# Kernel optimization log

Hardware: AMD Instinct MI355X
Metric: run time of the kernel (lower is better)

The kernel has to match this reference:

```python
import jax, jax.numpy as jnp
import numpy as np

K_OUT = 16  # k_out
DT = 0.1    # integration interval t=[0.0, 0.1], single rk4 step


def setup_inputs() -> dict:
    key = jax.random.key(0)
    ks = jax.random.split(key, 12)
    B, K_H, K_IN_TOT = 32768, 1024, 256
    s = 0.02
    return {
        "state": jax.random.normal(ks[0], (B, K_OUT + K_H), jnp.float32),
        "xt": jax.random.normal(ks[1], (B, K_IN_TOT), jnp.float32),
        "W1": jax.random.normal(ks[2], (K_H, 2 * K_H), jnp.float32) * s,
        "b1": jnp.zeros((2 * K_H,), jnp.float32),
        "W2": jax.random.normal(ks[3], (2 * K_H, K_H), jnp.float32) * s,
        "b2": jnp.zeros((K_H,), jnp.float32),
        "Wih": jax.random.normal(ks[4], (3 * K_H, K_IN_TOT), jnp.float32) * s,
        "Whh": jax.random.normal(ks[5], (3 * K_H, K_H), jnp.float32) * s,
        "bih": jnp.zeros((3 * K_H,), jnp.float32),
        "bhh": jnp.zeros((3 * K_H,), jnp.float32),
        "Wly": jax.random.normal(ks[6], (K_H, K_OUT), jnp.float32) * s,
        "bly": jnp.zeros((K_OUT,), jnp.float32),
        "y_type": jnp.zeros((K_OUT,), jnp.int32),  # 'd'/'s'/'n' all map to 0
    }


def _ode_f(h, W1, b1, W2, b2):
    # ODE_Rnn_Func: Linear -> Tanh -> Linear (time-independent)
    return jnp.tanh(h @ W1 + b1) @ W2 + b2


def _rk4_step(h, dt, W1, b1, W2, b2):
    k1 = _ode_f(h, W1, b1, W2, b2)
    k2 = _ode_f(h + 0.5 * dt * k1, W1, b1, W2, b2)
    k3 = _ode_f(h + 0.5 * dt * k2, W1, b1, W2, b2)
    k4 = _ode_f(h + dt * k3, W1, b1, W2, b2)
    return h + (dt / 6.0) * (k1 + 2.0 * k2 + 2.0 * k3 + k4)


def _gru_cell(x, h, Wih, Whh, bih, bhh):
    gi = x @ Wih.T + bih  # [B, 3*K_H]
    gh = h @ Whh.T + bhh
    i_r, i_z, i_n = jnp.split(gi, 3, axis=-1)
    h_r, h_z, h_n = jnp.split(gh, 3, axis=-1)
    r = jax.nn.sigmoid(i_r + h_r)
    z = jax.nn.sigmoid(i_z + h_z)
    n = jnp.tanh(i_n + r * h_n)
    return (1.0 - z) * n + z * h


def reference(state, xt, W1, b1, W2, b2, Wih, Whh, bih, bhh, Wly, bly, y_type):
    yt, ht = state[..., :K_OUT], state[..., K_OUT:]
    ht_ = _rk4_step(ht, DT, W1, b1, W2, b2)       # odeint(func, ht, [0, 0.1], method='rk4')[1]
    ht_new = _gru_cell(xt, ht_, Wih, Whh, bih, bhh)
    ly_out = ht_new @ Wly + bly                   # [B, K_OUT]
    mask = (y_type == 0)                          # all True for 'd'/'s'/'n'
    yt_new = jnp.where(mask, ly_out, yt)
    return jnp.concatenate([yt_new, ht_new], axis=-1)
```

## Files before the change

### kernel.cpp

```cpp
#include <hip/hip_runtime.h>
#include <hip/hip_fp8.h>
#include <cstdint>
#include <cstddef>

typedef __bf16 bf16_t;
typedef unsigned char fp8_t;
typedef __attribute__((ext_vector_type(8))) __bf16 bf16x8;
typedef __attribute__((ext_vector_type(4))) float f32x4;

__device__ __forceinline__ void async_cp16(const void* g, void* l) {
    __builtin_amdgcn_global_load_lds(
        (const __attribute__((address_space(1))) void*)g,
        (__attribute__((address_space(3))) void*)l,
        16, 0, 0);
}

__device__ __forceinline__ fp8_t to_fp8(float x) {
    __hip_fp8_e4m3 t(x);
    return t.__x;
}

__device__ __forceinline__ float fast_tanh(float x) {
    float ax = fabsf(x);
    float e = __expf(-2.f * ax);
    float t = (1.f - e) / (1.f + e);
    return x < 0.f ? -t : t;
}
__device__ __forceinline__ float fast_sig(float x) {
    return 1.f / (1.f + __expf(-x));
}

__global__ void k_cvt_transpose8(const float* __restrict__ src, fp8_t* __restrict__ dst,
                                 int K, int N) {
    int idx = blockIdx.x * 256 + threadIdx.x;
    if (idx >= K * N) return;
    int k = idx / N, n = idx - k * N;
    dst[(size_t)n * K + k] = to_fp8(src[idx]);
}

__global__ void k_cvt_flat(const float* __restrict__ src, bf16_t* __restrict__ dst, int n) {
    int idx = blockIdx.x * 256 + threadIdx.x;
    if (idx >= n) return;
    dst[idx] = (bf16_t)src[idx];
}

__global__ void k_build_wrz(const float* __restrict__ Wih, const float* __restrict__ Whh,
                            const float* __restrict__ bih, const float* __restrict__ bhh,
                            bf16_t* __restrict__ wrz, float* __restrict__ brz) {
    int idx = blockIdx.x * 256 + threadIdx.x;
    if (idx >= 2048 * 1280) return;
    int n = idx / 1280, c = idx - n * 1280;
    float v = (c < 256) ? Wih[(size_t)n * 256 + c] : Whh[(size_t)n * 1024 + (c - 256)];
    wrz[idx] = (bf16_t)v;
    if (c == 0) brz[n] = bih[n] + bhh[n];
}

__global__ void k_cvt_inputs(const float* __restrict__ xt, const float* __restrict__ state,
                             bf16_t* __restrict__ xh, bf16_t* __restrict__ h0b,
                             fp8_t* __restrict__ hs8, int B) {
    int idx = blockIdx.x * 256 + threadIdx.x;
    if (idx >= B * 1280) return;
    int b = idx / 1280, c = idx - b * 1280;
    if (c < 256) {
        xh[(size_t)b * 1280 + c] = (bf16_t)xt[(size_t)b * 256 + c];
    } else {
        int j = c - 256;
        float v = state[(size_t)b * 1040 + 16 + j];
        h0b[(size_t)b * 1024 + j] = (bf16_t)v;
        hs8[(size_t)b * 1024 + j] = to_fp8(v);
    }
}

enum { EPI_TANH = 0, EPI_RK4 = 1, EPI_SIG = 2, EPI_BIASBF = 3, EPI_FIN = 4 };

template <int EPI, int STAGE>
__global__ __launch_bounds__(512, 4) void gemm128f8(
    const fp8_t* __restrict__ A, int lda,
    const fp8_t* __restrict__ Bt,
    int N, int K,
    const float* __restrict__ bias,
    fp8_t* __restrict__ o8,
    const bf16_t* __restrict__ h0b,
    const float* __restrict__ state,
    bf16_t* __restrict__ kacc,
    bf16_t* __restrict__ xhb)
{
    __shared__ __align__(16) fp8_t dsA[3][8192];
    __shared__ __align__(16) fp8_t dsB[3][16384];

    const int tid  = threadIdx.x;
    const int lane = tid & 63;
    const int wv   = tid >> 6;

    const int gx  = gridDim.x;
    int bid = blockIdx.y * gx + blockIdx.x;
    const int nwg = gx * gridDim.y;
    bid = (bid & 7) * (nwg >> 3) + (bid >> 3);
    const int bm = (bid / gx) << 7;
    const int bn = (bid % gx) << 8;

    const int wm = (wv >> 2) << 6;
    const int wn = (wv & 3) << 6;

    f32x4 acc[4][4] = {};

    const int srow = tid >> 2;
    const int s4   = tid & 3;
    const int scol = ((s4 ^ ((srow >> 1) & 3)) << 4);
    const fp8_t* gA0 = A  + (size_t)(bm + srow) * lda + scol;
    const fp8_t* gB0 = Bt + (size_t)(bn + srow) * K + scol;
    const fp8_t* gB1 = gB0 + (size_t)128 * K;
    const int d0 = tid << 4;

#define STG(t) do { const int _sl = (t) % 3; const size_t _o = (size_t)(t) << 6; \
        async_cp16(gA0 + _o, (void*)&dsA[_sl][d0]);                              \
        async_cp16(gB0 + _o, (void*)&dsB[_sl][d0]);                              \
        async_cp16(gB1 + _o, (void*)&dsB[_sl][8192 + d0]); } while (0)

    const int fr  = lane & 15;
    const int kg  = lane >> 4;
    const int mS  = ((fr >> 1) & 3) << 1;
    const int aRow = (wm + fr) * 64;
    const int bRow = (wn + fr) * 64;
    const int sk0 = ((kg ^ mS) & 7) << 3;
    const int sk1 = (((4 | kg) ^ mS) & 7) << 3;

    const int NT = K >> 6;

    STG(0);
    STG(1);

    for (int kt = 0; kt < NT; ++kt) {
        if (kt + 1 < NT) asm volatile("s_waitcnt vmcnt(3)" ::: "memory");
        else             asm volatile("s_waitcnt vmcnt(0)" ::: "memory");
        __builtin_amdgcn_s_barrier();

        if (kt + 2 < NT) STG(kt + 2);

        const fp8_t* as = dsA[kt % 3];
        const fp8_t* bs = dsB[kt % 3];
        long a0[4], a1[4], b0[4], b1[4];
#pragma unroll
        for (int i = 0; i < 4; ++i) {
            a0[i] = *(const long*)(as + aRow + i * 1024 + sk0);
            a1[i] = *(const long*)(as + aRow + i * 1024 + sk1);
        }
#pragma unroll
        for (int j = 0; j < 4; ++j) {
            b0[j] = *(const long*)(bs + bRow + j * 1024 + sk0);
            b1[j] = *(const long*)(bs + bRow + j * 1024 + sk1);
        }

        __builtin_amdgcn_s_setprio(1);
#pragma unroll
        for (int i = 0; i < 4; ++i)
#pragma unroll
            for (int j = 0; j < 4; ++j)
                acc[i][j] = __builtin_amdgcn_mfma_f32_16x16x32_fp8_fp8(
                    a0[i], b0[j], acc[i][j], 0, 0, 0);
#pragma unroll
        for (int i = 0; i < 4; ++i)
#pragma unroll
            for (int j = 0; j < 4; ++j)
                acc[i][j] = __builtin_amdgcn_mfma_f32_16x16x32_fp8_fp8(
                    a1[i], b1[j], acc[i][j], 0, 0, 0);
        __builtin_amdgcn_s_setprio(0);
    }
#undef STG

    const int orow0 = bm + wm + (kg << 2);
    const int ocol0 = bn + wn + fr;
#pragma unroll
    for (int i = 0; i < 4; ++i) {
#pragma unroll
        for (int j = 0; j < 4; ++j) {
#pragma unroll
            for (int r = 0; r < 4; ++r) {
                const int row = orow0 + i * 16 + r;
                const int col = ocol0 + j * 16;
                const float c = acc[i][j][r];
                if constexpr (EPI == EPI_TANH) {
                    o8[(size_t)row * N + col] = to_fp8(fast_tanh(c + bias[col]));
                } else {
                    const float kk = c + bias[col];
                    const size_t hidx = ((size_t)row << 10) + col;
                    if constexpr (STAGE == 0) {
                        const float h0 = (float)h0b[hidx];
                        kacc[hidx] = (bf16_t)kk;
                        o8[hidx] = to_fp8(h0 + 0.05f * kk);
                    } else if constexpr (STAGE == 1) {
                        const float h0 = (float)h0b[hidx];
                        kacc[hidx] = (bf16_t)((float)kacc[hidx] + 2.f * kk);
                        o8[hidx] = to_fp8(h0 + 0.05f * kk);
                    } else if constexpr (STAGE == 2) {
                        const float h0 = (float)h0b[hidx];
                        kacc[hidx] = (bf16_t)((float)kacc[hidx] + 2.f * kk);
                        o8[hidx] = to_fp8(h0 + 0.1f * kk);
                    } else {
                        const float h0 = state[(size_t)row * 1040 + 16 + col];
                        const float ht = h0 + (0.1f / 6.f) * ((float)kacc[hidx] + kk);
                        xhb[(size_t)row * 1280 + col] = (bf16_t)ht;
                    }
                }
            }
        }
    }
}

template <int EPI>
__global__ __launch_bounds__(512, 4) void gemm128bf(
    const bf16_t* __restrict__ A, int lda,
    const bf16_t* __restrict__ Bt,
    int N, int K,
    const float* __restrict__ bias,
    bf16_t* __restrict__ o16,
    const bf16_t* __restrict__ rz,
    const bf16_t* __restrict__ inb,
    float* __restrict__ outp)
{
    __shared__ __align__(16) bf16_t As[3][4096];
    __shared__ __align__(16) bf16_t Bs[3][8192];

    const int tid  = threadIdx.x;
    const int lane = tid & 63;
    const int wv   = tid >> 6;

    const int gx  = gridDim.x;
    int bid = blockIdx.y * gx + blockIdx.x;
    const int nwg = gx * gridDim.y;
    if ((nwg & 7) == 0) bid = (bid & 7) * (nwg >> 3) + (bid >> 3);
    const int bm = (bid / gx) << 7;
    const int bn = (bid % gx) << 8;

    const int wm = (wv >> 2) << 6;
    const int wn = (wv & 3) << 6;

    f32x4 acc[4][4] = {};

    const int srow = tid >> 2;
    const int s4   = tid & 3;
    const int scw  = (s4 ^ ((srow >> 1) & 3)) << 3;
    const bf16_t* gA0 = A  + (size_t)(bm + srow) * lda + scw;
    const bf16_t* gB0 = Bt + (size_t)(bn + srow) * K + scw;
    const bf16_t* gB1 = gB0 + (size_t)128 * K;
    const int ldsOff = tid << 3;

#define STG(t) do { const int _sl = (t) % 3; const size_t _o = (size_t)(t) << 5; \
        async_cp16(gA0 + _o, (void*)&As[_sl][ldsOff]);                           \
        async_cp16(gB0 + _o, (void*)&Bs[_sl][ldsOff]);                           \
        async_cp16(gB1 + _o, (void*)&Bs[_sl][4096 + ldsOff]); } while (0)

    const int fr = lane & 15;
    const int kg = lane >> 4;
    const int ra = wm + fr;
    const int rb = wn + fr;
    const int aoff0 = ra * 32 + ((kg ^ ((ra >> 1) & 3)) << 3);
    const int boff0 = rb * 32 + ((kg ^ ((rb >> 1) & 3)) << 3);

    const int NT = K >> 5;

    STG(0);
    STG(1);

    for (int kt = 0; kt < NT; ++kt) {
        if (kt + 1 < NT) asm volatile("s_waitcnt vmcnt(3)" ::: "memory");
        else             asm volatile("s_waitcnt vmcnt(0)" ::: "memory");
        __builtin_amdgcn_s_barrier();

        if (kt + 2 < NT) STG(kt + 2);

        const bf16_t* as = &As[kt % 3][0];
        const bf16_t* bs = &Bs[kt % 3][0];
        bf16x8 af[4], bfr[4];
#pragma unroll
        for (int i = 0; i < 4; ++i) af[i]  = *(const bf16x8*)(as + aoff0 + i * 512);
#pragma unroll
        for (int j = 0; j < 4; ++j) bfr[j] = *(const bf16x8*)(bs + boff0 + j * 512);

        __builtin_amdgcn_s_setprio(1);
#pragma unroll
        for (int i = 0; i < 4; ++i)
#pragma unroll
            for (int j = 0; j < 4; ++j)
                acc[i][j] = __builtin_amdgcn_mfma_f32_16x16x32_bf16(af[i], bfr[j], acc[i][j], 0, 0, 0);
        __builtin_amdgcn_s_setprio(0);
    }
#undef STG

    const int orow0 = bm + wm + (kg << 2);
    const int ocol0 = bn + wn + fr;
#pragma unroll
    for (int i = 0; i < 4; ++i) {
#pragma unroll
        for (int j = 0; j < 4; ++j) {
#pragma unroll
            for (int r = 0; r < 4; ++r) {
                const int row = orow0 + i * 16 + r;
                const int col = ocol0 + j * 16;
                const float c = acc[i][j][r];
                if constexpr (EPI == EPI_SIG) {
                    o16[(size_t)row * N + col] = (bf16_t)fast_sig(c + bias[col]);
                } else if constexpr (EPI == EPI_BIASBF) {
                    o16[(size_t)row * N + col] = (bf16_t)(c + bias[col]);
                } else {
                    const float hn  = c + bias[col];
                    const float r_  = (float)rz[((size_t)row << 11) + col];
                    const float z_  = (float)rz[((size_t)row << 11) + 1024 + col];
                    const float inv = (float)inb[((size_t)row << 10) + col];
                    const float nn  = fast_tanh(inv + r_ * hn);
                    const float htv = (float)A[(size_t)row * lda + col];
                    outp[(size_t)row * 1040 + 16 + col] = (1.f - z_) * nn + z_ * htv;
                }
            }
        }
    }
}

__global__ void k_ly(const float* __restrict__ outh, const float* __restrict__ state,
                     const float* __restrict__ Wly, const float* __restrict__ bly,
                     const int* __restrict__ y_type, float* __restrict__ outp, int B) {
    int t = blockIdx.x * 256 + threadIdx.x;
    if (t >= B * 16) return;
    int o = t & 15, b = t >> 4;
    const float4* hrow = (const float4*)(outh + (size_t)b * 1040 + 16);
    float s = bly[o];
#pragma unroll 4
    for (int k4 = 0; k4 < 256; ++k4) {
        float4 h = hrow[k4];
        int k = k4 << 2;
        s += h.x * Wly[(k + 0) * 16 + o] + h.y * Wly[(k + 1) * 16 + o]
           + h.z * Wly[(k + 2) * 16 + o] + h.w * Wly[(k + 3) * 16 + o];
    }
    outp[(size_t)b * 1040 + o] = (y_type[o] == 0) ? s : state[(size_t)b * 1040 + o];
}

extern "C" void kernel_launch(void* const* d_in, const int* in_sizes, int n_in,
                              void* d_out, int out_size, void* d_ws, size_t ws_size,
                              hipStream_t stream) {
    const float* state = (const float*)d_in[0];
    const float* xt    = (const float*)d_in[1];
    const float* W1    = (const float*)d_in[2];
    const float* b1    = (const float*)d_in[3];
    const float* W2    = (const float*)d_in[4];
    const float* b2    = (const float*)d_in[5];
    const float* Wih   = (const float*)d_in[6];
    const float* Whh   = (const float*)d_in[7];
    const float* bih   = (const float*)d_in[8];
    const float* bhh   = (const float*)d_in[9];
    const float* Wly   = (const float*)d_in[10];
    const float* bly   = (const float*)d_in[11];
    const int*   y_type = (const int*)d_in[12];
    float* out = (float*)d_out;

    const int B = in_sizes[0] / 1040;

    char* ws = (char*)d_ws;
    fp8_t*  w1t8 = (fp8_t*) (ws);
    fp8_t*  w2t8 = (fp8_t*) (ws + 2097152);
    bf16_t* wrz  = (bf16_t*)(ws + 4194304);
    bf16_t* win  = (bf16_t*)(ws + 9437184);
    bf16_t* whn  = (bf16_t*)(ws + 9961472);
    float*  brz  = (float*) (ws + 12058624);
    bf16_t* xh   = (bf16_t*)(ws + 12066816);
    fp8_t*  hs8  = (fp8_t*) (ws + 95952896);
    bf16_t* kacc = (bf16_t*)(ws + 129507328);
    fp8_t*  T8   = (fp8_t*) (ws + 196616192);
    bf16_t* h0b  = (bf16_t*)(ws + 263725056);
    bf16_t* rz   = (bf16_t*)(ws + 196616192);
    bf16_t* inb  = (bf16_t*)(ws + 95952896);

    k_cvt_transpose8<<<(1024 * 2048) / 256, 256, 0, stream>>>(W1, w1t8, 1024, 2048);
    k_cvt_transpose8<<<(2048 * 1024) / 256, 256, 0, stream>>>(W2, w2t8, 2048, 1024);
    k_build_wrz<<<(2048 * 1280) / 256, 256, 0, stream>>>(Wih, Whh, bih, bhh, wrz, brz);
    k_cvt_flat<<<(1024 * 256) / 256, 256, 0, stream>>>(Wih + 2048 * 256, win, 1024 * 256);
    k_cvt_flat<<<(1024 * 1024) / 256, 256, 0, stream>>>(Whh + 2048 * 1024, whn, 1024 * 1024);
    k_cvt_inputs<<<(B * 1280) / 256, 256, 0, stream>>>(xt, state, xh, h0b, hs8, B);

    const int MB = B / 128;

    gemm128f8<EPI_TANH, 0><<<dim3(8, MB), 512, 0, stream>>>(hs8, 1024, w1t8, 2048, 1024,
        b1, T8, nullptr, nullptr, nullptr, nullptr);
    gemm128f8<EPI_RK4, 0><<<dim3(4, MB), 512, 0, stream>>>(T8, 2048, w2t8, 1024, 2048,
        b2, hs8, h0b, nullptr, kacc, nullptr);

    gemm128f8<EPI_TANH, 0><<<dim3(8, MB), 512, 0, stream>>>(hs8, 1024, w1t8, 2048, 1024,
        b1, T8, nullptr, nullptr, nullptr, nullptr);
    gemm128f8<EPI_RK4, 1><<<dim3(4, MB), 512, 0, stream>>>(T8, 2048, w2t8, 1024, 2048,
        b2, hs8, h0b, nullptr, kacc, nullptr);

    gemm128f8<EPI_TANH, 0><<<dim3(8, MB), 512, 0, stream>>>(hs8, 1024, w1t8, 2048, 1024,
        b1, T8, nullptr, nullptr, nullptr, nullptr);
    gemm128f8<EPI_RK4, 2><<<dim3(4, MB), 512, 0, stream>>>(T8, 2048, w2t8, 1024, 2048,
        b2, hs8, h0b, nullptr, kacc, nullptr);

    gemm128f8<EPI_TANH, 0><<<dim3(8, MB), 512, 0, stream>>>(hs8, 1024, w1t8, 2048, 1024,
        b1, T8, nullptr, nullptr, nullptr, nullptr);
    gemm128f8<EPI_RK4, 3><<<dim3(4, MB), 512, 0, stream>>>(T8, 2048, w2t8, 1024, 2048,
        b2, nullptr, nullptr, state, kacc, xh + 256);

    gemm128bf<EPI_SIG><<<dim3(8, MB), 512, 0, stream>>>(xh, 1280, wrz, 2048, 1280,
        brz, rz, nullptr, nullptr, nullptr);
    gemm128bf<EPI_BIASBF><<<dim3(4, MB), 512, 0, stream>>>(xh, 1280, win, 1024, 256,
        bih + 2048, inb, nullptr, nullptr, nullptr);
    gemm128bf<EPI_FIN><<<dim3(4, MB), 512, 0, stream>>>(xh + 256, 1280, whn, 1024, 1024,
        bhh + 2048, nullptr, rz, inb, out);

    k_ly<<<(B * 16) / 256, 256, 0, stream>>>(out, state, Wly, bly, y_type, out, B);
}
```

Before: 1.852 ms.

## Grow GEMM block tile to 256x256 with 1024-thread workgroups

Both the FP8 and BF16 GEMM kernels move from 128x256 tiles with 512 threads to 256x256 tiles with 1024 threads (16 waves). The A staging buffer doubles and each thread now issues one A and one B async copy per stage, so the vmcnt wait drops from 3 to 2. The aim is more operand reuse per tile and less global/L2 traffic for the B matrix. The trade-off is twice the LDS per block, which lowers how many blocks fit on a CU, and only half as many blocks across the grid. The launch_bounds occupancy hint of 4 blocks per CU is unlikely to be met at 1024 threads.

```diff
diff --git a/kernel.cpp b/kernel.cpp
--- a/kernel.cpp
+++ b/kernel.cpp
@@ -74,7 +74,7 @@
 enum { EPI_TANH = 0, EPI_RK4 = 1, EPI_SIG = 2, EPI_BIASBF = 3, EPI_FIN = 4 };
 
 template <int EPI, int STAGE>
-__global__ __launch_bounds__(512, 4) void gemm128f8(
+__global__ __launch_bounds__(1024, 4) void gemm256f8(
     const fp8_t* __restrict__ A, int lda,
     const fp8_t* __restrict__ Bt,
     int N, int K,
@@ -85,7 +85,7 @@
     bf16_t* __restrict__ kacc,
     bf16_t* __restrict__ xhb)
 {
-    __shared__ __align__(16) fp8_t dsA[3][8192];
+    __shared__ __align__(16) fp8_t dsA[3][16384];
     __shared__ __align__(16) fp8_t dsB[3][16384];
 
     const int tid  = threadIdx.x;
@@ -96,7 +96,7 @@
     int bid = blockIdx.y * gx + blockIdx.x;
     const int nwg = gx * gridDim.y;
     bid = (bid & 7) * (nwg >> 3) + (bid >> 3);
-    const int bm = (bid / gx) << 7;
+    const int bm = (bid / gx) << 8;
     const int bn = (bid % gx) << 8;
 
     const int wm = (wv >> 2) << 6;
@@ -109,13 +109,11 @@
     const int scol = ((s4 ^ ((srow >> 1) & 3)) << 4);
     const fp8_t* gA0 = A  + (size_t)(bm + srow) * lda + scol;
     const fp8_t* gB0 = Bt + (size_t)(bn + srow) * K + scol;
-    const fp8_t* gB1 = gB0 + (size_t)128 * K;
     const int d0 = tid << 4;
 
 #define STG(t) do { const int _sl = (t) % 3; const size_t _o = (size_t)(t) << 6; \
         async_cp16(gA0 + _o, (void*)&dsA[_sl][d0]);                              \
-        async_cp16(gB0 + _o, (void*)&dsB[_sl][d0]);                              \
-        async_cp16(gB1 + _o, (void*)&dsB[_sl][8192 + d0]); } while (0)
+        async_cp16(gB0 + _o, (void*)&dsB[_sl][d0]); } while (0)
 
     const int fr  = lane & 15;
     const int kg  = lane >> 4;
@@ -131,7 +129,7 @@
     STG(1);
 
     for (int kt = 0; kt < NT; ++kt) {
-        if (kt + 1 < NT) asm volatile("s_waitcnt vmcnt(3)" ::: "memory");
+        if (kt + 1 < NT) asm volatile("s_waitcnt vmcnt(2)" ::: "memory");
         else             asm volatile("s_waitcnt vmcnt(0)" ::: "memory");
         __builtin_amdgcn_s_barrier();
 
@@ -208,7 +206,7 @@
 }
 
 template <int EPI>
-__global__ __launch_bounds__(512, 4) void gemm128bf(
+__global__ __launch_bounds__(1024, 4) void gemm256bf(
     const bf16_t* __restrict__ A, int lda,
     const bf16_t* __restrict__ Bt,
     int N, int K,
@@ -218,7 +216,7 @@
     const bf16_t* __restrict__ inb,
     float* __restrict__ outp)
 {
-    __shared__ __align__(16) bf16_t As[3][4096];
+    __shared__ __align__(16) bf16_t As[3][8192];
     __shared__ __align__(16) bf16_t Bs[3][8192];
 
     const int tid  = threadIdx.x;
@@ -229,7 +227,7 @@
     int bid = blockIdx.y * gx + blockIdx.x;
     const int nwg = gx * gridDim.y;
     if ((nwg & 7) == 0) bid = (bid & 7) * (nwg >> 3) + (bid >> 3);
-    const int bm = (bid / gx) << 7;
+    const int bm = (bid / gx) << 8;
     const int bn = (bid % gx) << 8;
 
     const int wm = (wv >> 2) << 6;
@@ -242,13 +240,11 @@
     const int scw  = (s4 ^ ((srow >> 1) & 3)) << 3;
     const bf16_t* gA0 = A  + (size_t)(bm + srow) * lda + scw;
     const bf16_t* gB0 = Bt + (size_t)(bn + srow) * K + scw;
-    const bf16_t* gB1 = gB0 + (size_t)128 * K;
     const int ldsOff = tid << 3;
 
 #define STG(t) do { const int _sl = (t) % 3; const size_t _o = (size_t)(t) << 5; \
         async_cp16(gA0 + _o, (void*)&As[_sl][ldsOff]);                           \
-        async_cp16(gB0 + _o, (void*)&Bs[_sl][ldsOff]);                           \
-        async_cp16(gB1 + _o, (void*)&Bs[_sl][4096 + ldsOff]); } while (0)
+        async_cp16(gB0 + _o, (void*)&Bs[_sl][ldsOff]); } while (0)
 
     const int fr = lane & 15;
     const int kg = lane >> 4;
@@ -263,7 +259,7 @@
     STG(1);
 
     for (int kt = 0; kt < NT; ++kt) {
-        if (kt + 1 < NT) asm volatile("s_waitcnt vmcnt(3)" ::: "memory");
+        if (kt + 1 < NT) asm volatile("s_waitcnt vmcnt(2)" ::: "memory");
         else             asm volatile("s_waitcnt vmcnt(0)" ::: "memory");
         __builtin_amdgcn_s_barrier();
 
@@ -376,33 +372,33 @@
     k_cvt_flat<<<(1024 * 1024) / 256, 256, 0, stream>>>(Whh + 2048 * 1024, whn, 1024 * 1024);
     k_cvt_inputs<<<(B * 1280) / 256, 256, 0, stream>>>(xt, state, xh, h0b, hs8, B);
 
-    const int MB = B / 128;
-
-    gemm128f8<EPI_TANH, 0><<<dim3(8, MB), 512, 0, stream>>>(hs8, 1024, w1t8, 2048, 1024,
+    const int MB = B / 256;
+
+    gemm256f8<EPI_TANH, 0><<<dim3(8, MB), 1024, 0, stream>>>(hs8, 1024, w1t8, 2048, 1024,
         b1, T8, nullptr, nullptr, nullptr, nullptr);
-    gemm128f8<EPI_RK4, 0><<<dim3(4, MB), 512, 0, stream>>>(T8, 2048, w2t8, 1024, 2048,
+    gemm256f8<EPI_RK4, 0><<<dim3(4, MB), 1024, 0, stream>>>(T8, 2048, w2t8, 1024, 2048,
         b2, hs8, h0b, nullptr, kacc, nullptr);
 
-    gemm128f8<EPI_TANH, 0><<<dim3(8, MB), 512, 0, stream>>>(hs8, 1024, w1t8, 2048, 1024,
+    gemm256f8<EPI_TANH, 0><<<dim3(8, MB), 1024, 0, stream>>>(hs8, 1024, w1t8, 2048, 1024,
         b1, T8, nullptr, nullptr, nullptr, nullptr);
-    gemm128f8<EPI_RK4, 1><<<dim3(4, MB), 512, 0, stream>>>(T8, 2048, w2t8, 1024, 2048,
+    gemm256f8<EPI_RK4, 1><<<dim3(4, MB), 1024, 0, stream>>>(T8, 2048, w2t8, 1024, 2048,
         b2, hs8, h0b, nullptr, kacc, nullptr);
 
-    gemm128f8<EPI_TANH, 0><<<dim3(8, MB), 512, 0, stream>>>(hs8, 1024, w1t8, 2048, 1024,
+    gemm256f8<EPI_TANH, 0><<<dim3(8, MB), 1024, 0, stream>>>(hs8, 1024, w1t8, 2048, 1024,
         b1, T8, nullptr, nullptr, nullptr, nullptr);
-    gemm128f8<EPI_RK4, 2><<<dim3(4, MB), 512, 0, stream>>>(T8, 2048, w2t8, 1024, 2048,
+    gemm256f8<EPI_RK4, 2><<<dim3(4, MB), 1024, 0, stream>>>(T8, 2048, w2t8, 1024, 2048,
         b2, hs8, h0b, nullptr, kacc, nullptr);
 
-    gemm128f8<EPI_TANH, 0><<<dim3(8, MB), 512, 0, stream>>>(hs8, 1024, w1t8, 2048, 1024,
+    gemm256f8<EPI_TANH, 0><<<dim3(8, MB), 1024, 0, stream>>>(hs8, 1024, w1t8, 2048, 1024,
         b1, T8, nullptr, nullptr, nullptr, nullptr);
-    gemm128f8<EPI_RK4, 3><<<dim3(4, MB), 512, 0, stream>>>(T8, 2048, w2t8, 1024, 2048,
+    gemm256f8<EPI_RK4, 3><<<dim3(4, MB), 1024, 0, stream>>>(T8, 2048, w2t8, 1024, 2048,
         b2, nullptr, nullptr, state, kacc, xh + 256);
 
-    gemm128bf<EPI_SIG><<<dim3(8, MB), 512, 0, stream>>>(xh, 1280, wrz, 2048, 1280,
+    gemm256bf<EPI_SIG><<<dim3(8, MB), 1024, 0, stream>>>(xh, 1280, wrz, 2048, 1280,
         brz, rz, nullptr, nullptr, nullptr);
-    gemm128bf<EPI_BIASBF><<<dim3(4, MB), 512, 0, stream>>>(xh, 1280, win, 1024, 256,
+    gemm256bf<EPI_BIASBF><<<dim3(4, MB), 1024, 0, stream>>>(xh, 1280, win, 1024, 256,
         bih + 2048, inb, nullptr, nullptr, nullptr);
-    gemm128bf<EPI_FIN><<<dim3(4, MB), 512, 0, stream>>>(xh + 256, 1280, whn, 1024, 1024,
+    gemm256bf<EPI_FIN><<<dim3(4, MB), 1024, 0, stream>>>(xh + 256, 1280, whn, 1024, 1024,
         bhh + 2048, nullptr, rz, inb, out);
 
     k_ly<<<(B * 16) / 256, 256, 0, stream>>>(out, state, Wly, bly, y_type, out, B);
```

Result: slower. 2.034 ms (+9.8%).
